# Kernel tuning notes

Measured on AMD Instinct MI355X. Metric: run time of the kernel, lower is better.

The kernel has to match this reference:

```python
import jax, jax.numpy as jnp
import numpy as np

HIDDEN = 4096
N_HEADS = 32
N_KV_HEADS = 8
HEAD_DIM = 128
ROPE_THETA = 1e6
RMS_EPS = 1e-6
SEQ = 2048


def setup_inputs() -> dict:
    key = jax.random.key(0)
    k1, k2, k3 = jax.random.split(key, 3)
    hidden_states = jax.random.normal(k1, (SEQ, HIDDEN), dtype=jnp.float32)
    # fused QKV weight: [hidden, (H + 2*Hkv) * head_dim]
    qkv_out = (N_HEADS + 2 * N_KV_HEADS) * HEAD_DIM
    w_qkv = jax.random.normal(k2, (HIDDEN, qkv_out), dtype=jnp.float32) * (HIDDEN ** -0.5)
    w_o = jax.random.normal(k3, (N_HEADS * HEAD_DIM, HIDDEN), dtype=jnp.float32) * ((N_HEADS * HEAD_DIM) ** -0.5)
    q_norm_w = jnp.ones((HEAD_DIM,), dtype=jnp.float32)
    k_norm_w = jnp.ones((HEAD_DIM,), dtype=jnp.float32)
    # NeoX-style rotary tables [T, head_dim/2]
    pos = jnp.arange(SEQ, dtype=jnp.float32)
    inv_freq = 1.0 / (ROPE_THETA ** (jnp.arange(0, HEAD_DIM, 2, dtype=jnp.float32) / HEAD_DIM))
    freqs = pos[:, None] * inv_freq[None, :]  # [T, d/2]
    cos = jnp.cos(freqs)
    sin = jnp.sin(freqs)
    return {"hidden_states": hidden_states, "cos": cos, "sin": sin,
            "w_qkv": w_qkv, "w_o": w_o, "q_norm_w": q_norm_w, "k_norm_w": k_norm_w}


def _rms_norm(x, w, eps=RMS_EPS):
    # per-head RMSNorm over last dim (head_dim)
    var = jnp.mean(jnp.square(x), axis=-1, keepdims=True)
    return x * jax.lax.rsqrt(var + eps) * w


def _rope(x, cos, sin):
    # NeoX rotate-half: x split into two halves of head_dim
    d2 = x.shape[-1] // 2
    x1, x2 = x[..., :d2], x[..., d2:]
    c = cos[:, None, :]  # [T,1,d/2] broadcast over heads
    s = sin[:, None, :]
    return jnp.concatenate([x1 * c - x2 * s, x2 * c + x1 * s], axis=-1)


def reference(hidden_states, cos, sin, w_qkv, w_o, q_norm_w, k_norm_w):
    T = hidden_states.shape[0]
    H, Hkv, D = N_HEADS, N_KV_HEADS, HEAD_DIM
    G = H // Hkv  # GQA group size
    scale = D ** -0.5

    qkv = hidden_states @ w_qkv  # [T, (H+2Hkv)*D]
    q, k, v = jnp.split(qkv, [H * D, (H + Hkv) * D], axis=1)
    q = q.reshape(T, H, D)
    k = k.reshape(T, Hkv, D)
    v = v.reshape(T, Hkv, D)

    q = _rms_norm(q, q_norm_w)
    k = _rms_norm(k, k_norm_w)
    q = _rope(q, cos, sin)
    k = _rope(k, cos, sin)

    # GQA: group query heads onto shared KV heads
    qg = q.reshape(T, Hkv, G, D)
    scores = jnp.einsum('qhgd,khd->hgqk', qg, k) * scale  # [Hkv,G,T,T]
    causal = jnp.tril(jnp.ones((T, T), dtype=bool))
    scores = jnp.where(causal, scores, jnp.float32(-1e30))
    probs = jax.nn.softmax(scores, axis=-1)
    out = jnp.einsum('hgqk,khd->qhgd', probs, v).reshape(T, H * D)
    return out @ w_o  # [T, hidden]
```

## Files before the change

kernel.cpp:

```cpp
#include <hip/hip_runtime.h>
#include <stdint.h>

#define SEQ   2048
#define HID   4096
#define NQH   32
#define NKVH  8
#define HD    128
#define QKVN  6144

typedef uint16_t u16;
typedef __attribute__((ext_vector_type(8))) short bf16x8;
typedef __attribute__((ext_vector_type(4))) float f32x4;
typedef __attribute__((ext_vector_type(4))) unsigned int u32x4;

static __device__ __forceinline__ float bf2f(u16 h){
  union { float f; unsigned int u; } v; v.u = ((unsigned int)h) << 16; return v.f;
}
static __device__ __forceinline__ u16 f2bf(float f){
  unsigned int u = __float_as_uint(f);
  return (u16)((u + 0x7fffu + ((u >> 16) & 1u)) >> 16);
}
static __device__ __forceinline__ f32x4 mfma16(bf16x8 a, bf16x8 b, f32x4 c){
  return __builtin_amdgcn_mfma_f32_16x16x32_bf16(a, b, c, 0, 0, 0);
}
static __device__ __forceinline__ void gload16(const void* g, void* l){
  __builtin_amdgcn_global_load_lds((const __attribute__((address_space(1))) void*)g,
                                   (__attribute__((address_space(3))) void*)l, 16, 0, 0);
}

__global__ void k_cvt(const float* __restrict__ src, u16* __restrict__ dst, int n4){
  int i = blockIdx.x * blockDim.x + threadIdx.x;
  if (i >= n4) return;
  float4 v = ((const float4*)src)[i];
  uint2 o;
  o.x = (unsigned)f2bf(v.x) | ((unsigned)f2bf(v.y) << 16);
  o.y = (unsigned)f2bf(v.z) | ((unsigned)f2bf(v.w) << 16);
  ((uint2*)dst)[i] = o;
}

__global__ void k_addf(const float* __restrict__ a, float* __restrict__ o, int n4){
  int i = blockIdx.x * blockDim.x + threadIdx.x;
  if (i >= n4) return;
  float4 x = ((const float4*)o)[i];
  float4 y = ((const float4*)a)[i];
  x.x += y.x; x.y += y.y; x.z += y.z; x.w += y.w;
  ((float4*)o)[i] = x;
}

__global__ void k_transpose_cvt(const float* __restrict__ src, u16* __restrict__ dst, int K, int N){
  __shared__ float t[32][33];
  int n0 = blockIdx.x * 32, k0 = blockIdx.y * 32;
  int tx = threadIdx.x, ty = threadIdx.y;
#pragma unroll
  for (int i = 0; i < 32; i += 8)
    t[ty + i][tx] = src[(size_t)(k0 + ty + i) * N + n0 + tx];
  __syncthreads();
#pragma unroll
  for (int i = 0; i < 32; i += 8)
    dst[(size_t)(n0 + ty + i) * K + k0 + tx] = f2bf(t[tx][ty + i]);
}

__global__ __launch_bounds__(512) void k_gemm192(const u16* __restrict__ A, const u16* __restrict__ Bt,
                                                 u16* __restrict__ Cv, int M, int N, int K){
  __shared__ __align__(16) u16 Asm[2][256][64];
  __shared__ __align__(16) u16 Bsm[2][192][64];
  const int tid = threadIdx.x, lane = tid & 63, wid = tid >> 6;
  const int wm = wid >> 2, wn = wid & 3;
  const int l16 = lane & 15, lhi = lane >> 4;
  const int rx = l16 & 7;
  const int bid = blockIdx.x;
  const int xcd = bid & 7, jj = bid >> 3;
  const size_t bcol = (size_t)(xcd * 4 + jj % 4) * 192;
  const size_t brow = (size_t)((jj / 4) & 7) * 256;

  const f32x4 vz = {0.f, 0.f, 0.f, 0.f};
  f32x4 acc[8][3];
#pragma unroll
  for (int m = 0; m < 8; m++)
#pragma unroll
    for (int n = 0; n < 3; n++) acc[m][n] = vz;

  const int srow = lane >> 3;
  const int sg   = (lane & 7) ^ srow;
  const u16* Ags = A  + (brow + wid*8 + srow) * (size_t)K + sg*8;
  const u16* Bgs = Bt + (bcol + wid*8 + srow) * (size_t)K + sg*8;
  const int NT = K >> 6, NU = NT >> 1;

#define FRA(buf, mi, kh) (*(const bf16x8*)&Asm[buf][wm*128 + (mi)*16 + l16][(((kh)*4 + lhi) ^ rx) << 3])
#define FRB(buf, ni, kh) (*(const bf16x8*)&Bsm[buf][wn*48 + (ni)*16 + l16][(((kh)*4 + lhi) ^ rx) << 3])
#define STG_A(tile, half) do{ if ((tile) < NT){                                  \
    const size_t ko_ = (size_t)((half)*128) * K + (size_t)(tile) * 64;           \
    gload16(Ags + ko_,                &Asm[(tile)&1][(half)*128 + wid*8][0]);     \
    gload16(Ags + ko_ + (size_t)64*K, &Asm[(tile)&1][(half)*128 + 64 + wid*8][0]); } }while(0)
#define STG_B(tile, r) do{ if ((tile) < NT){                                     \
    const size_t ko_ = (size_t)((r)*64) * K + (size_t)(tile) * 64;               \
    gload16(Bgs + ko_, &Bsm[(tile)&1][(r)*64 + wid*8][0]); } }while(0)

  STG_B(0,0); STG_B(0,1); STG_B(0,2);
  STG_A(0,0); STG_A(0,1);
  STG_B(1,0); STG_B(1,1); STG_B(1,2);
  asm volatile("s_waitcnt vmcnt(3)" ::: "memory");
  __builtin_amdgcn_sched_barrier(0);
  __builtin_amdgcn_s_barrier();

  bf16x8 fA[4][2], fB01[2][2], fB2[2];
  for (int u = 0; u < NU; ++u){
    const int t = 2 * u;
#pragma unroll
    for (int mi = 0; mi < 4; ++mi){ fA[mi][0] = FRA(0, mi, 0); fA[mi][1] = FRA(0, mi, 1); }
#pragma unroll
    for (int ni = 0; ni < 2; ++ni){ fB01[ni][0] = FRB(0, ni, 0); fB01[ni][1] = FRB(0, ni, 1); }
    STG_A(t + 1, 0);
    asm volatile("s_waitcnt lgkmcnt(8)" ::: "memory");
    __builtin_amdgcn_s_barrier();
    asm volatile("s_waitcnt lgkmcnt(0)" ::: "memory");
    __builtin_amdgcn_sched_barrier(0);
    __builtin_amdgcn_s_setprio(1);
#pragma unroll
    for (int kh = 0; kh < 2; ++kh)
#pragma unroll
      for (int mi = 0; mi < 4; ++mi)
#pragma unroll
        for (int ni = 0; ni < 2; ++ni)
          acc[mi][ni] = mfma16(fA[mi][kh], fB01[ni][kh], acc[mi][ni]);
    __builtin_amdgcn_s_setprio(0);
    __builtin_amdgcn_s_barrier();
    fB2[0] = FRB(0, 2, 0); fB2[1] = FRB(0, 2, 1);
    STG_A(t + 1, 1);
    __builtin_amdgcn_s_barrier();
    asm volatile("s_waitcnt lgkmcnt(0)" ::: "memory");
    __builtin_amdgcn_sched_barrier(0);
    __builtin_amdgcn_s_setprio(1);
#pragma unroll
    for (int kh = 0; kh < 2; ++kh)
#pragma unroll
      for (int mi = 0; mi < 4; ++mi)
        acc[mi][2] = mfma16(fA[mi][kh], fB2[kh], acc[mi][2]);
    __builtin_amdgcn_s_setprio(0);
    __builtin_amdgcn_s_barrier();
#pragma unroll
    for (int mi = 0; mi < 4; ++mi){ fA[mi][0] = FRA(0, 4 + mi, 0); fA[mi][1] = FRA(0, 4 + mi, 1); }
    STG_B(t + 2, 0);
    __builtin_amdgcn_s_barrier();
    asm volatile("s_waitcnt lgkmcnt(0)" ::: "memory");
    __builtin_amdgcn_sched_barrier(0);
    __builtin_amdgcn_s_setprio(1);
#pragma unroll
    for (int kh = 0; kh < 2; ++kh)
#pragma unroll
      for (int mi = 0; mi < 4; ++mi)
#pragma unroll
        for (int ni = 0; ni < 2; ++ni)
          acc[4 + mi][ni] = mfma16(fA[mi][kh], fB01[ni][kh], acc[4 + mi][ni]);
    __builtin_amdgcn_s_setprio(0);
    __builtin_amdgcn_s_barrier();
    STG_B(t + 2, 1); STG_B(t + 2, 2);
    __builtin_amdgcn_s_barrier();
    asm volatile("s_waitcnt lgkmcnt(0)" ::: "memory");
    __builtin_amdgcn_sched_barrier(0);
    __builtin_amdgcn_s_setprio(1);
#pragma unroll
    for (int kh = 0; kh < 2; ++kh)
#pragma unroll
      for (int mi = 0; mi < 4; ++mi)
        acc[4 + mi][2] = mfma16(fA[mi][kh], fB2[kh], acc[4 + mi][2]);
    __builtin_amdgcn_s_setprio(0);
    if (u == NU - 1) asm volatile("s_waitcnt vmcnt(0)" ::: "memory");
    else             asm volatile("s_waitcnt vmcnt(3)" ::: "memory");
    __builtin_amdgcn_sched_barrier(0);
    __builtin_amdgcn_s_barrier();
#pragma unroll
    for (int mi = 0; mi < 4; ++mi){ fA[mi][0] = FRA(1, mi, 0); fA[mi][1] = FRA(1, mi, 1); }
#pragma unroll
    for (int ni = 0; ni < 2; ++ni){ fB01[ni][0] = FRB(1, ni, 0); fB01[ni][1] = FRB(1, ni, 1); }
    STG_A(t + 2, 0);
    asm volatile("s_waitcnt lgkmcnt(8)" ::: "memory");
    __builtin_amdgcn_s_barrier();
    asm volatile("s_waitcnt lgkmcnt(0)" ::: "memory");
    __builtin_amdgcn_sched_barrier(0);
    __builtin_amdgcn_s_setprio(1);
#pragma unroll
    for (int kh = 0; kh < 2; ++kh)
#pragma unroll
      for (int mi = 0; mi < 4; ++mi)
#pragma unroll
        for (int ni = 0; ni < 2; ++ni)
          acc[mi][ni] = mfma16(fA[mi][kh], fB01[ni][kh], acc[mi][ni]);
    __builtin_amdgcn_s_setprio(0);
    __builtin_amdgcn_s_barrier();
    fB2[0] = FRB(1, 2, 0); fB2[1] = FRB(1, 2, 1);
    STG_A(t + 2, 1);
    __builtin_amdgcn_s_barrier();
    asm volatile("s_waitcnt lgkmcnt(0)" ::: "memory");
    __builtin_amdgcn_sched_barrier(0);
    __builtin_amdgcn_s_setprio(1);
#pragma unroll
    for (int kh = 0; kh < 2; ++kh)
#pragma unroll
      for (int mi = 0; mi < 4; ++mi)
        acc[mi][2] = mfma16(fA[mi][kh], fB2[kh], acc[mi][2]);
    __builtin_amdgcn_s_setprio(0);
    __builtin_amdgcn_s_barrier();
#pragma unroll
    for (int mi = 0; mi < 4; ++mi){ fA[mi][0] = FRA(1, 4 + mi, 0); fA[mi][1] = FRA(1, 4 + mi, 1); }
    STG_B(t + 3, 0);
    __builtin_amdgcn_s_barrier();
    asm volatile("s_waitcnt lgkmcnt(0)" ::: "memory");
    __builtin_amdgcn_sched_barrier(0);
    __builtin_amdgcn_s_setprio(1);
#pragma unroll
    for (int kh = 0; kh < 2; ++kh)
#pragma unroll
      for (int mi = 0; mi < 4; ++mi)
#pragma unroll
        for (int ni = 0; ni < 2; ++ni)
          acc[4 + mi][ni] = mfma16(fA[mi][kh], fB01[ni][kh], acc[4 + mi][ni]);
    __builtin_amdgcn_s_setprio(0);
    __builtin_amdgcn_s_barrier();
    STG_B(t + 3, 1); STG_B(t + 3, 2);
    __builtin_amdgcn_s_barrier();
    asm volatile("s_waitcnt lgkmcnt(0)" ::: "memory");
    __builtin_amdgcn_sched_barrier(0);
    __builtin_amdgcn_s_setprio(1);
#pragma unroll
    for (int kh = 0; kh < 2; ++kh)
#pragma unroll
      for (int mi = 0; mi < 4; ++mi)
        acc[4 + mi][2] = mfma16(fA[mi][kh], fB2[kh], acc[4 + mi][2]);
    __builtin_amdgcn_s_setprio(0);
    asm volatile("s_waitcnt vmcnt(3)" ::: "memory");
    __builtin_amdgcn_sched_barrier(0);
    __builtin_amdgcn_s_barrier();
  }
#undef FRA
#undef FRB
#undef STG_A
#undef STG_B

#pragma unroll
  for (int mi = 0; mi < 8; mi++)
#pragma unroll
    for (int ni = 0; ni < 3; ni++)
#pragma unroll
      for (int i = 0; i < 4; i++){
        size_t row = brow + wm*128 + mi*16 + lhi*4 + i;
        size_t col = bcol + wn*48 + ni*16 + l16;
        Cv[row * (size_t)N + col] = f2bf(acc[mi][ni][i]);
      }
}

template<int OUTBF, int SPLITK, int XBC, int NBY>
__global__ __launch_bounds__(512) void k_gemm(const u16* __restrict__ A, const u16* __restrict__ Bt,
                                              void* __restrict__ Cv0, void* __restrict__ Cv1,
                                              int M, int N, int K){
  __shared__ __align__(16) u16 Asm[2][2][128][64];
  __shared__ __align__(16) u16 Bsm[2][2][128][64];
  const int tid = threadIdx.x, lane = tid & 63, wid = tid >> 6;
  const int wm = wid >> 2, wn = wid & 3;
  const int l16 = lane & 15, lhi = lane >> 4;
  const int rx = l16 & 7;
  const int bid = blockIdx.x;
  const int xcd = bid & 7, jj = bid >> 3;
  const int bcol_i = xcd * XBC + jj % XBC;
  const int rest = jj / XBC;
  const int brow_i = rest % NBY;
  const int kz = (SPLITK > 1) ? (rest / NBY) : 0;
  const size_t brow = (size_t)brow_i * 256, bcol = (size_t)bcol_i * 256;
  const int kbeg = kz * (K / SPLITK);
  void* Cv = (kz == 0) ? Cv0 : Cv1;

  const f32x4 vz = {0.f, 0.f, 0.f, 0.f};
  f32x4 acc[8][4];
#pragma unroll
  for (int m = 0; m < 8; m++)
#pragma unroll
    for (int n = 0; n < 4; n++) acc[m][n] = vz;

  const int srow = lane >> 3;
  const int sg   = (lane & 7) ^ srow;
  const u16* Ags = A  + (brow + wid*8 + srow) * (size_t)K + sg*8 + kbeg;
  const u16* Bgs = Bt + (bcol + wid*8 + srow) * (size_t)K + sg*8 + kbeg;
  const int NT = (K / SPLITK) >> 6;
  const int NU = NT >> 1;

#define FRA(buf, mi, kh) (*(const bf16x8*)&Asm[buf][wm][(mi)*16 + l16][(((kh)*4 + lhi) ^ rx) << 3])
#define FRB(buf, ni, kh) (*(const bf16x8*)&Bsm[buf][wn >> 1][(wn & 1)*64 + (ni)*16 + l16][(((kh)*4 + lhi) ^ rx) << 3])
#define STG_A(tile, half) do{ if ((tile) < NT){                                  \
    const size_t ko_ = (size_t)((half)*128) * K + (size_t)(tile) * 64;           \
    gload16(Ags + ko_,                &Asm[(tile)&1][half][wid*8][0]);           \
    gload16(Ags + ko_ + (size_t)64*K, &Asm[(tile)&1][half][64 + wid*8][0]); } }while(0)
#define STG_B(tile, half) do{ if ((tile) < NT){                                  \
    const size_t ko_ = (size_t)((half)*128) * K + (size_t)(tile) * 64;           \
    gload16(Bgs + ko_,                &Bsm[(tile)&1][half][wid*8][0]);           \
    gload16(Bgs + ko_ + (size_t)64*K, &Bsm[(tile)&1][half][64 + wid*8][0]); } }while(0)

  STG_B(0, 0); STG_B(0, 1); STG_A(0, 0); STG_A(0, 1); STG_B(1, 0); STG_B(1, 1);
  asm volatile("s_waitcnt vmcnt(4)" ::: "memory");
  __builtin_amdgcn_sched_barrier(0);
  __builtin_amdgcn_s_barrier();

  bf16x8 fA[4][2], fB01[2][2], fB23[2][2];
  for (int u = 0; u < NU; ++u){
    const int t = 2 * u;
#pragma unroll
    for (int mi = 0; mi < 4; ++mi){ fA[mi][0] = FRA(0, mi, 0); fA[mi][1] = FRA(0, mi, 1); }
#pragma unroll
    for (int ni = 0; ni < 2; ++ni){ fB01[ni][0] = FRB(0, ni, 0); fB01[ni][1] = FRB(0, ni, 1); }
    STG_A(t + 1, 0);
    asm volatile("s_waitcnt lgkmcnt(8)" ::: "memory");
    __builtin_amdgcn_s_barrier();
    asm volatile("s_waitcnt lgkmcnt(0)" ::: "memory");
    __builtin_amdgcn_sched_barrier(0);
    __builtin_amdgcn_s_setprio(1);
#pragma unroll
    for (int kh = 0; kh < 2; ++kh)
#pragma unroll
      for (int mi = 0; mi < 4; ++mi)
#pragma unroll
        for (int ni = 0; ni < 2; ++ni)
          acc[mi][ni] = mfma16(fA[mi][kh], fB01[ni][kh], acc[mi][ni]);
    __builtin_amdgcn_s_setprio(0);
    __builtin_amdgcn_s_barrier();
#pragma unroll
    for (int ni = 0; ni < 2; ++ni){ fB23[ni][0] = FRB(0, 2 + ni, 0); fB23[ni][1] = FRB(0, 2 + ni, 1); }
    STG_A(t + 1, 1);
    __builtin_amdgcn_s_barrier();
    asm volatile("s_waitcnt lgkmcnt(0)" ::: "memory");
    __builtin_amdgcn_sched_barrier(0);
    __builtin_amdgcn_s_setprio(1);
#pragma unroll
    for (int kh = 0; kh < 2; ++kh)
#pragma unroll
      for (int mi = 0; mi < 4; ++mi)
#pragma unroll
        for (int ni = 0; ni < 2; ++ni)
          acc[mi][2 + ni] = mfma16(fA[mi][kh], fB23[ni][kh], acc[mi][2 + ni]);
    __builtin_amdgcn_s_setprio(0);
    __builtin_amdgcn_s_barrier();
#pragma unroll
    for (int mi = 0; mi < 4; ++mi){ fA[mi][0] = FRA(0, 4 + mi, 0); fA[mi][1] = FRA(0, 4 + mi, 1); }
    STG_B(t + 2, 0);
    __builtin_amdgcn_s_barrier();
    asm volatile("s_waitcnt lgkmcnt(0)" ::: "memory");
    __builtin_amdgcn_sched_barrier(0);
    __builtin_amdgcn_s_setprio(1);
#pragma unroll
    for (int kh = 0; kh < 2; ++kh)
#pragma unroll
      for (int mi = 0; mi < 4; ++mi)
#pragma unroll
        for (int ni = 0; ni < 2; ++ni)
          acc[4 + mi][ni] = mfma16(fA[mi][kh], fB01[ni][kh], acc[4 + mi][ni]);
    __builtin_amdgcn_s_setprio(0);
    __builtin_amdgcn_s_barrier();
    STG_B(t + 2, 1);
    __builtin_amdgcn_s_barrier();
    asm volatile("s_waitcnt lgkmcnt(0)" ::: "memory");
    __builtin_amdgcn_sched_barrier(0);
    __builtin_amdgcn_s_setprio(1);
#pragma unroll
    for (int kh = 0; kh < 2; ++kh)
#pragma unroll
      for (int mi = 0; mi < 4; ++mi)
#pragma unroll
        for (int ni = 0; ni < 2; ++ni)
          acc[4 + mi][2 + ni] = mfma16(fA[mi][kh], fB23[ni][kh], acc[4 + mi][2 + ni]);
    __builtin_amdgcn_s_setprio(0);
    if (u == NU - 1) asm volatile("s_waitcnt vmcnt(0)" ::: "memory");
    else             asm volatile("s_waitcnt vmcnt(4)" ::: "memory");
    __builtin_amdgcn_sched_barrier(0);
    __builtin_amdgcn_s_barrier();
#pragma unroll
    for (int mi = 0; mi < 4; ++mi){ fA[mi][0] = FRA(1, mi, 0); fA[mi][1] = FRA(1, mi, 1); }
#pragma unroll
    for (int ni = 0; ni < 2; ++ni){ fB01[ni][0] = FRB(1, ni, 0); fB01[ni][1] = FRB(1, ni, 1); }
    STG_A(t + 2, 0);
    asm volatile("s_waitcnt lgkmcnt(8)" ::: "memory");
    __builtin_amdgcn_s_barrier();
    asm volatile("s_waitcnt lgkmcnt(0)" ::: "memory");
    __builtin_amdgcn_sched_barrier(0);
    __builtin_amdgcn_s_setprio(1);
#pragma unroll
    for (int kh = 0; kh < 2; ++kh)
#pragma unroll
      for (int mi = 0; mi < 4; ++mi)
#pragma unroll
        for (int ni = 0; ni < 2; ++ni)
          acc[mi][ni] = mfma16(fA[mi][kh], fB01[ni][kh], acc[mi][ni]);
    __builtin_amdgcn_s_setprio(0);
    __builtin_amdgcn_s_barrier();
#pragma unroll
    for (int ni = 0; ni < 2; ++ni){ fB23[ni][0] = FRB(1, 2 + ni, 0); fB23[ni][1] = FRB(1, 2 + ni, 1); }
    STG_A(t + 2, 1);
    __builtin_amdgcn_s_barrier();
    asm volatile("s_waitcnt lgkmcnt(0)" ::: "memory");
    __builtin_amdgcn_sched_barrier(0);
    __builtin_amdgcn_s_setprio(1);
#pragma unroll
    for (int kh = 0; kh < 2; ++kh)
#pragma unroll
      for (int mi = 0; mi < 4; ++mi)
#pragma unroll
        for (int ni = 0; ni < 2; ++ni)
          acc[mi][2 + ni] = mfma16(fA[mi][kh], fB23[ni][kh], acc[mi][2 + ni]);
    __builtin_amdgcn_s_setprio(0);
    __builtin_amdgcn_s_barrier();
#pragma unroll
    for (int mi = 0; mi < 4; ++mi){ fA[mi][0] = FRA(1, 4 + mi, 0); fA[mi][1] = FRA(1, 4 + mi, 1); }
    STG_B(t + 3, 0);
    __builtin_amdgcn_s_barrier();
    asm volatile("s_waitcnt lgkmcnt(0)" ::: "memory");
    __builtin_amdgcn_sched_barrier(0);
    __builtin_amdgcn_s_setprio(1);
#pragma unroll
    for (int kh = 0; kh < 2; ++kh)
#pragma unroll
      for (int mi = 0; mi < 4; ++mi)
#pragma unroll
        for (int ni = 0; ni < 2; ++ni)
          acc[4 + mi][ni] = mfma16(fA[mi][kh], fB01[ni][kh], acc[4 + mi][ni]);
    __builtin_amdgcn_s_setprio(0);
    __builtin_amdgcn_s_barrier();
    STG_B(t + 3, 1);
    __builtin_amdgcn_s_barrier();
    asm volatile("s_waitcnt lgkmcnt(0)" ::: "memory");
    __builtin_amdgcn_sched_barrier(0);
    __builtin_amdgcn_s_setprio(1);
#pragma unroll
    for (int kh = 0; kh < 2; ++kh)
#pragma unroll
      for (int mi = 0; mi < 4; ++mi)
#pragma unroll
        for (int ni = 0; ni < 2; ++ni)
          acc[4 + mi][2 + ni] = mfma16(fA[mi][kh], fB23[ni][kh], acc[4 + mi][2 + ni]);
    __builtin_amdgcn_s_setprio(0);
    asm volatile("s_waitcnt vmcnt(4)" ::: "memory");
    __builtin_amdgcn_sched_barrier(0);
    __builtin_amdgcn_s_barrier();
  }
#undef FRA
#undef FRB
#undef STG_A
#undef STG_B

#pragma unroll
  for (int mi = 0; mi < 8; mi++)
#pragma unroll
    for (int ni = 0; ni < 4; ni++)
#pragma unroll
      for (int i = 0; i < 4; i++){
        size_t row = brow + wm*128 + mi*16 + lhi*4 + i;
        size_t col = bcol + wn*64 + ni*16 + l16;
        if (OUTBF) ((u16*)Cv)[row * (size_t)N + col] = f2bf(acc[mi][ni][i]);
        else       ((float*)Cv)[row * (size_t)N + col] = acc[mi][ni][i];
      }
}

__global__ __launch_bounds__(256) void k_rmsrope(const u16* __restrict__ qkv, const float* __restrict__ cosp,
                                                 const float* __restrict__ sinp, const float* __restrict__ qw,
                                                 const float* __restrict__ kw, u16* __restrict__ Qr,
                                                 u16* __restrict__ Kr){
  int t = blockIdx.x;
  int lane = threadIdx.x & 63, w = threadIdx.x >> 6;
  int hh = blockIdx.y * 4 + w;
  bool isq = hh < NQH;
  int hl = isq ? hh : hh - NQH;
  const u16* src = qkv + (size_t)t * QKVN + (isq ? hl * HD : NQH * HD + hl * HD);
  unsigned u = *(const unsigned*)(src + 2 * lane);
  float x0 = bf2f((u16)(u & 0xffffu)), x1 = bf2f((u16)(u >> 16));
  float ss = x0 * x0 + x1 * x1;
#pragma unroll
  for (int m = 1; m < 64; m <<= 1) ss += __shfl_xor(ss, m);
  float rs = rsqrtf(ss * (1.f / HD) + 1e-6f);
  const float* wp = isq ? qw : kw;
  float w0 = wp[2 * lane], w1 = wp[2 * lane + 1];
  float xn0 = x0 * rs * w0, xn1 = x1 * rs * w1;
  float p0 = __shfl_xor(xn0, 32), p1 = __shfl_xor(xn1, 32);
  int j0 = (2 * lane) & 63;
  float c0 = cosp[t * 64 + j0], c1 = cosp[t * 64 + j0 + 1];
  float s0 = sinp[t * 64 + j0], s1 = sinp[t * 64 + j0 + 1];
  float o0, o1;
  if (lane < 32){ o0 = xn0 * c0 - p0 * s0; o1 = xn1 * c1 - p1 * s1; }
  else          { o0 = xn0 * c0 + p0 * s0; o1 = xn1 * c1 + p1 * s1; }
  if (isq){ o0 *= 0.08838834764831845f; o1 *= 0.08838834764831845f; }
  u16* dst = isq ? (Qr + ((size_t)hl * SEQ + t) * HD) : (Kr + ((size_t)hl * SEQ + t) * HD);
  *(unsigned*)(dst + 2 * lane) = (unsigned)f2bf(o0) | ((unsigned)f2bf(o1) << 16);
}

__global__ void k_vt(const u16* __restrict__ qkv, u16* __restrict__ VT){
  __shared__ u16 t[32][33];
  int t0 = blockIdx.x * 32, d0 = blockIdx.y * 32, hv = blockIdx.z;
  int tx = threadIdx.x, ty = threadIdx.y;
#pragma unroll
  for (int i = 0; i < 32; i += 8)
    t[ty + i][tx] = qkv[(size_t)(t0 + ty + i) * QKVN + (NQH + NKVH) * HD + hv * HD + d0 + tx];
  __syncthreads();
#pragma unroll
  for (int i = 0; i < 32; i += 8)
    VT[((size_t)hv * HD + d0 + ty + i) * SEQ + t0 + tx] = t[tx][ty + i];
}

__global__ __launch_bounds__(512) void k_attn(const u16* __restrict__ Q, const u16* __restrict__ Kg,
                                              const u16* __restrict__ VTg, u16* __restrict__ AO){
  __shared__ __align__(16) u16 Ksm[2][128][128];
  __shared__ __align__(16) u16 Vsm[128][128];
  __shared__ __align__(16) u16 Psm[8][16][136];
  int tid = threadIdx.x, lane = tid & 63, wid = tid >> 6;
  int l16 = lane & 15, lhi = lane >> 4;
  int bid = blockIdx.x;
  int kvg = bid & 7, rr = bid >> 3;
  int J = 7 - (rr >> 2);
  int hq = kvg * 4 + (rr & 3);
  int qb = J * 256;
  const u16* Kh = Kg  + (size_t)kvg * SEQ * HD;
  const u16* Vh = VTg + (size_t)kvg * HD * SEQ;
  const u16* Qh = Q   + (size_t)hq * SEQ * HD;

  bf16x8 qf[2][4];
#pragma unroll
  for (int m = 0; m < 2; m++)
#pragma unroll
    for (int ks = 0; ks < 4; ks++)
      qf[m][ks] = *(const bf16x8*)(Qh + (size_t)(qb + wid*32 + m*16 + l16) * HD + ks*32 + lhi*8);

  const f32x4 vz = {0.f, 0.f, 0.f, 0.f};
  f32x4 o[2][8];
  float mrow[2][4], lrow[2][4];
#pragma unroll
  for (int m = 0; m < 2; m++){
#pragma unroll
    for (int n = 0; n < 8; n++) o[m][n] = vz;
#pragma unroll
    for (int i = 0; i < 4; i++){ mrow[m][i] = -1e30f; lrow[m][i] = 0.f; }
  }

  int rsub = lane >> 4, g = lane & 15;
  const u16 *Ks0, *Ks1, *Ks2, *Ks3, *Vs0, *Vs1, *Vs2, *Vs3;
  {
    int r0 = wid*16 + 0*4 + rsub, r1 = wid*16 + 1*4 + rsub;
    int r2 = wid*16 + 2*4 + rsub, r3 = wid*16 + 3*4 + rsub;
    Ks0 = Kh + (size_t)r0 * HD + ((g ^ (r0 & 7)) << 3);
    Ks1 = Kh + (size_t)r1 * HD + ((g ^ (r1 & 7)) << 3);
    Ks2 = Kh + (size_t)r2 * HD + ((g ^ (r2 & 7)) << 3);
    Ks3 = Kh + (size_t)r3 * HD + ((g ^ (r3 & 7)) << 3);
    Vs0 = Vh + (size_t)r0 * SEQ + ((g ^ (r0 & 7)) << 3);
    Vs1 = Vh + (size_t)r1 * SEQ + ((g ^ (r1 & 7)) << 3);
    Vs2 = Vh + (size_t)r2 * SEQ + ((g ^ (r2 & 7)) << 3);
    Vs3 = Vh + (size_t)r3 * SEQ + ((g ^ (r3 & 7)) << 3);
  }

  gload16(Ks0, &Ksm[0][wid*16 +  0][0]);
  gload16(Ks1, &Ksm[0][wid*16 +  4][0]);
  gload16(Ks2, &Ksm[0][wid*16 +  8][0]);
  gload16(Ks3, &Ksm[0][wid*16 + 12][0]);
  asm volatile("s_waitcnt vmcnt(0)" ::: "memory");
  __builtin_amdgcn_sched_barrier(0);
  __builtin_amdgcn_s_barrier();

  int ntr = 2*J + 2;
  int wbase = qb + wid*32;
  for (int t = 0; t < ntr; t++){
    int cur = t & 1, nxt = cur ^ 1;
    int kt0 = t << 7;
    bool pf = (t + 1 < ntr);
    gload16(Vs0 + kt0, &Vsm[wid*16 +  0][0]);
    gload16(Vs1 + kt0, &Vsm[wid*16 +  4][0]);
    gload16(Vs2 + kt0, &Vsm[wid*16 +  8][0]);
    gload16(Vs3 + kt0, &Vsm[wid*16 + 12][0]);
    if (pf){
      size_t ko = (size_t)(kt0 + 128) * HD;
      gload16(Ks0 + ko, &Ksm[nxt][wid*16 +  0][0]);
      gload16(Ks1 + ko, &Ksm[nxt][wid*16 +  4][0]);
      gload16(Ks2 + ko, &Ksm[nxt][wid*16 +  8][0]);
      gload16(Ks3 + ko, &Ksm[nxt][wid*16 + 12][0]);
    }
    bool act = (kt0 <= wbase + 31);
    f32x4 s[2][8];
    if (act){
#pragma unroll
      for (int m = 0; m < 2; m++)
#pragma unroll
        for (int n = 0; n < 8; n++) s[m][n] = vz;
      const u16* kbase = &Ksm[cur][0][0];
      __builtin_amdgcn_s_setprio(1);
#pragma unroll
      for (int n = 0; n < 8; n++){
        int row = n*16 + l16, rxk = row & 7;
#pragma unroll
        for (int ks = 0; ks < 4; ks++){
          bf16x8 kf = *(const bf16x8*)(kbase + row*128 + (((ks*4 + lhi) ^ rxk) << 3));
          s[0][n] = mfma16(qf[0][ks], kf, s[0][n]);
          s[1][n] = mfma16(qf[1][ks], kf, s[1][n]);
        }
      }
      __builtin_amdgcn_s_setprio(0);
      if (kt0 + 127 > wbase){
#pragma unroll
        for (int m = 0; m < 2; m++)
#pragma unroll
          for (int n = 0; n < 8; n++)
#pragma unroll
            for (int i = 0; i < 4; i++)
              if (kt0 + n*16 + l16 > wbase + m*16 + lhi*4 + i) s[m][n][i] = -1e30f;
      }
#pragma unroll
      for (int m = 0; m < 2; m++)
#pragma unroll
        for (int i = 0; i < 4; i++){
          float tm = fmaxf(fmaxf(fmaxf(s[m][0][i], s[m][1][i]), fmaxf(s[m][2][i], s[m][3][i])),
                           fmaxf(fmaxf(s[m][4][i], s[m][5][i]), fmaxf(s[m][6][i], s[m][7][i])));
          tm = fmaxf(tm, __shfl_xor(tm, 1));
          tm = fmaxf(tm, __shfl_xor(tm, 2));
          tm = fmaxf(tm, __shfl_xor(tm, 4));
          tm = fmaxf(tm, __shfl_xor(tm, 8));
          float nm = fmaxf(mrow[m][i], tm);
          float sc = __expf(mrow[m][i] - nm);
          mrow[m][i] = nm;
          float rsum = 0.f;
#pragma unroll
          for (int n = 0; n < 8; n++){
            float p = __expf(s[m][n][i] - nm);
            s[m][n][i] = p;
            rsum += p;
          }
          rsum += __shfl_xor(rsum, 1);
          rsum += __shfl_xor(rsum, 2);
          rsum += __shfl_xor(rsum, 4);
          rsum += __shfl_xor(rsum, 8);
          lrow[m][i] = lrow[m][i] * sc + rsum;
#pragma unroll
          for (int n = 0; n < 8; n++) o[m][n][i] *= sc;
        }
    }
    if (pf) asm volatile("s_waitcnt vmcnt(4)" ::: "memory");
    else    asm volatile("s_waitcnt vmcnt(0)" ::: "memory");
    __builtin_amdgcn_sched_barrier(0);
    __builtin_amdgcn_s_barrier();
    __builtin_amdgcn_sched_barrier(0);
    if (act){
      bf16x8 pa0[4], pa1[4];
#pragma unroll
      for (int n = 0; n < 8; n++)
#pragma unroll
        for (int i = 0; i < 4; i++)
          Psm[wid][lhi*4 + i][n*16 + l16] = f2bf(s[0][n][i]);
#pragma unroll
      for (int ksv = 0; ksv < 4; ksv++)
        pa0[ksv] = *(const bf16x8*)&Psm[wid][l16][ksv*32 + lhi*8];
      __builtin_amdgcn_sched_barrier(0);
#pragma unroll
      for (int n = 0; n < 8; n++)
#pragma unroll
        for (int i = 0; i < 4; i++)
          Psm[wid][lhi*4 + i][n*16 + l16] = f2bf(s[1][n][i]);
#pragma unroll
      for (int ksv = 0; ksv < 4; ksv++)
        pa1[ksv] = *(const bf16x8*)&Psm[wid][l16][ksv*32 + lhi*8];
      __builtin_amdgcn_s_setprio(1);
#pragma unroll
      for (int ksv = 0; ksv < 4; ksv++){
#pragma unroll
        for (int n = 0; n < 8; n++){
          int row = n*16 + l16;
          bf16x8 vb = *(const bf16x8*)(&Vsm[0][0] + row*128 + (((ksv*4 + lhi) ^ (row & 7)) << 3));
          o[0][n] = mfma16(pa0[ksv], vb, o[0][n]);
          o[1][n] = mfma16(pa1[ksv], vb, o[1][n]);
        }
      }
      __builtin_amdgcn_s_setprio(0);
    }
    asm volatile("s_waitcnt vmcnt(0)" ::: "memory");
    __builtin_amdgcn_sched_barrier(0);
    __builtin_amdgcn_s_barrier();
  }
#pragma unroll
  for (int m = 0; m < 2; m++){
    float inv[4];
#pragma unroll
    for (int i = 0; i < 4; i++) inv[i] = 1.f / lrow[m][i];
#pragma unroll
    for (int n = 0; n < 8; n++)
#pragma unroll
      for (int i = 0; i < 4; i++){
        int trow = wbase + m*16 + lhi*4 + i;
        AO[(size_t)trow * HID + hq * HD + n*16 + l16] = f2bf(o[m][n][i] * inv[i]);
      }
  }
}

extern "C" void kernel_launch(void* const* d_in, const int* in_sizes, int n_in,
                              void* d_out, int out_size, void* d_ws, size_t ws_size,
                              hipStream_t stream){
  const float* hs   = (const float*)d_in[0];
  const float* cosp = (const float*)d_in[1];
  const float* sinp = (const float*)d_in[2];
  const float* wqkv = (const float*)d_in[3];
  const float* wo   = (const float*)d_in[4];
  const float* qw   = (const float*)d_in[5];
  const float* kw   = (const float*)d_in[6];
  float* out = (float*)d_out;
  char* ws = (char*)d_ws;
  u16* XB    = (u16*)(ws + 0);
  u16* WQKVT = (u16*)(ws + 16777216);
  u16* WOT   = (u16*)(ws + 0);
  float* SCR = (float*)(ws + 33554432);
  u16* QKV   = (u16*)(ws + 67108864);
  u16* QR    = (u16*)(ws + 92274688);
  u16* KR    = (u16*)(ws + 109051904);
  u16* VTB   = (u16*)(ws + 113246208);
  u16* AOB   = (u16*)(ws + 117440512);

  k_cvt<<<(SEQ * HID / 4 + 255) / 256, 256, 0, stream>>>(hs, XB, SEQ * HID / 4);
  k_transpose_cvt<<<dim3(QKVN / 32, HID / 32), dim3(32, 8), 0, stream>>>(wqkv, WQKVT, HID, QKVN);
  k_gemm192<<<256, 512, 0, stream>>>(XB, WQKVT, QKV, SEQ, QKVN, HID);
  k_transpose_cvt<<<dim3(HID / 32, HID / 32), dim3(32, 8), 0, stream>>>(wo, WOT, HID, HID);
  k_rmsrope<<<dim3(SEQ, 10), 256, 0, stream>>>(QKV, cosp, sinp, qw, kw, QR, KR);
  k_vt<<<dim3(SEQ / 32, HD / 32, NKVH), dim3(32, 8), 0, stream>>>(QKV, VTB);
  k_attn<<<256, 512, 0, stream>>>(QR, KR, VTB, AOB);
  k_gemm<0, 2, 2, 8><<<256, 512, 0, stream>>>(AOB, WOT, out, SCR, SEQ, HID, HID);
  k_addf<<<SEQ * HID / 4 / 256, 256, 0, stream>>>(SCR, out, SEQ * HID / 4);
}
```

Before: 374.9 us.

## Halve attention query tile to 128 rows and launch 512 blocks

The attention kernel now gives each block 128 query rows (16 per wave) instead of 256, and the grid grows from 256 to 512 blocks. Causal work per block is more even, and every wave now works on every KV tile, so the per-wave active flag goes away. P is written to shared memory before the barrier. Each K/V tile loaded from global memory is now used by half as many query rows, so total K/V traffic roughly doubles and there are fewer MFMAs per loaded fragment.

```diff
diff --git a/kernel.cpp b/kernel.cpp
--- a/kernel.cpp
+++ b/kernel.cpp
@@ -509,30 +509,25 @@
   int l16 = lane & 15, lhi = lane >> 4;
   int bid = blockIdx.x;
   int kvg = bid & 7, rr = bid >> 3;
-  int J = 7 - (rr >> 2);
+  int J = 15 - (rr >> 2);
   int hq = kvg * 4 + (rr & 3);
-  int qb = J * 256;
+  int qb = J * 128;
   const u16* Kh = Kg  + (size_t)kvg * SEQ * HD;
   const u16* Vh = VTg + (size_t)kvg * HD * SEQ;
   const u16* Qh = Q   + (size_t)hq * SEQ * HD;
 
-  bf16x8 qf[2][4];
-#pragma unroll
-  for (int m = 0; m < 2; m++)
-#pragma unroll
-    for (int ks = 0; ks < 4; ks++)
-      qf[m][ks] = *(const bf16x8*)(Qh + (size_t)(qb + wid*32 + m*16 + l16) * HD + ks*32 + lhi*8);
+  bf16x8 qf[4];
+#pragma unroll
+  for (int ks = 0; ks < 4; ks++)
+    qf[ks] = *(const bf16x8*)(Qh + (size_t)(qb + wid*16 + l16) * HD + ks*32 + lhi*8);
 
   const f32x4 vz = {0.f, 0.f, 0.f, 0.f};
-  f32x4 o[2][8];
-  float mrow[2][4], lrow[2][4];
-#pragma unroll
-  for (int m = 0; m < 2; m++){
-#pragma unroll
-    for (int n = 0; n < 8; n++) o[m][n] = vz;
-#pragma unroll
-    for (int i = 0; i < 4; i++){ mrow[m][i] = -1e30f; lrow[m][i] = 0.f; }
-  }
+  f32x4 o[8];
+  float mrow[4], lrow[4];
+#pragma unroll
+  for (int n = 0; n < 8; n++) o[n] = vz;
+#pragma unroll
+  for (int i = 0; i < 4; i++){ mrow[i] = -1e30f; lrow[i] = 0.f; }
 
   int rsub = lane >> 4, g = lane & 15;
   const u16 *Ks0, *Ks1, *Ks2, *Ks3, *Vs0, *Vs1, *Vs2, *Vs3;
@@ -557,8 +552,8 @@
   __builtin_amdgcn_sched_barrier(0);
   __builtin_amdgcn_s_barrier();
 
-  int ntr = 2*J + 2;
-  int wbase = qb + wid*32;
+  int ntr = J + 1;
+  int wrow0 = qb + wid*16;
   for (int t = 0; t < ntr; t++){
     int cur = t & 1, nxt = cur ^ 1;
     int kt0 = t << 7;
@@ -574,118 +569,90 @@
       gload16(Ks2 + ko, &Ksm[nxt][wid*16 +  8][0]);
       gload16(Ks3 + ko, &Ksm[nxt][wid*16 + 12][0]);
     }
-    bool act = (kt0 <= wbase + 31);
-    f32x4 s[2][8];
-    if (act){
-#pragma unroll
-      for (int m = 0; m < 2; m++)
-#pragma unroll
-        for (int n = 0; n < 8; n++) s[m][n] = vz;
-      const u16* kbase = &Ksm[cur][0][0];
-      __builtin_amdgcn_s_setprio(1);
+    f32x4 s[8];
+#pragma unroll
+    for (int n = 0; n < 8; n++) s[n] = vz;
+    const u16* kbase = &Ksm[cur][0][0];
+    __builtin_amdgcn_s_setprio(1);
+#pragma unroll
+    for (int n = 0; n < 8; n++){
+      int row = n*16 + l16, rxk = row & 7;
+#pragma unroll
+      for (int ks = 0; ks < 4; ks++){
+        bf16x8 kf = *(const bf16x8*)(kbase + row*128 + (((ks*4 + lhi) ^ rxk) << 3));
+        s[n] = mfma16(qf[ks], kf, s[n]);
+      }
+    }
+    __builtin_amdgcn_s_setprio(0);
+    if (kt0 + 127 > wrow0){
+#pragma unroll
+      for (int n = 0; n < 8; n++)
+#pragma unroll
+        for (int i = 0; i < 4; i++)
+          if (kt0 + n*16 + l16 > wrow0 + lhi*4 + i) s[n][i] = -1e30f;
+    }
+#pragma unroll
+    for (int i = 0; i < 4; i++){
+      float tm = fmaxf(fmaxf(fmaxf(s[0][i], s[1][i]), fmaxf(s[2][i], s[3][i])),
+                       fmaxf(fmaxf(s[4][i], s[5][i]), fmaxf(s[6][i], s[7][i])));
+      tm = fmaxf(tm, __shfl_xor(tm, 1));
+      tm = fmaxf(tm, __shfl_xor(tm, 2));
+      tm = fmaxf(tm, __shfl_xor(tm, 4));
+      tm = fmaxf(tm, __shfl_xor(tm, 8));
+      float nm = fmaxf(mrow[i], tm);
+      float sc = __expf(mrow[i] - nm);
+      mrow[i] = nm;
+      float rsum = 0.f;
 #pragma unroll
       for (int n = 0; n < 8; n++){
-        int row = n*16 + l16, rxk = row & 7;
-#pragma unroll
-        for (int ks = 0; ks < 4; ks++){
-          bf16x8 kf = *(const bf16x8*)(kbase + row*128 + (((ks*4 + lhi) ^ rxk) << 3));
-          s[0][n] = mfma16(qf[0][ks], kf, s[0][n]);
-          s[1][n] = mfma16(qf[1][ks], kf, s[1][n]);
-        }
+        float p = __expf(s[n][i] - nm);
+        s[n][i] = p;
+        rsum += p;
       }
-      __builtin_amdgcn_s_setprio(0);
-      if (kt0 + 127 > wbase){
-#pragma unroll
-        for (int m = 0; m < 2; m++)
-#pragma unroll
-          for (int n = 0; n < 8; n++)
-#pragma unroll
-            for (int i = 0; i < 4; i++)
-              if (kt0 + n*16 + l16 > wbase + m*16 + lhi*4 + i) s[m][n][i] = -1e30f;
-      }
-#pragma unroll
-      for (int m = 0; m < 2; m++)
-#pragma unroll
-        for (int i = 0; i < 4; i++){
-          float tm = fmaxf(fmaxf(fmaxf(s[m][0][i], s[m][1][i]), fmaxf(s[m][2][i], s[m][3][i])),
-                           fmaxf(fmaxf(s[m][4][i], s[m][5][i]), fmaxf(s[m][6][i], s[m][7][i])));
-          tm = fmaxf(tm, __shfl_xor(tm, 1));
-          tm = fmaxf(tm, __shfl_xor(tm, 2));
-          tm = fmaxf(tm, __shfl_xor(tm, 4));
-          tm = fmaxf(tm, __shfl_xor(tm, 8));
-          float nm = fmaxf(mrow[m][i], tm);
-          float sc = __expf(mrow[m][i] - nm);
-          mrow[m][i] = nm;
-          float rsum = 0.f;
-#pragma unroll
-          for (int n = 0; n < 8; n++){
-            float p = __expf(s[m][n][i] - nm);
-            s[m][n][i] = p;
-            rsum += p;
-          }
-          rsum += __shfl_xor(rsum, 1);
-          rsum += __shfl_xor(rsum, 2);
-          rsum += __shfl_xor(rsum, 4);
-          rsum += __shfl_xor(rsum, 8);
-          lrow[m][i] = lrow[m][i] * sc + rsum;
-#pragma unroll
-          for (int n = 0; n < 8; n++) o[m][n][i] *= sc;
-        }
+      rsum += __shfl_xor(rsum, 1);
+      rsum += __shfl_xor(rsum, 2);
+      rsum += __shfl_xor(rsum, 4);
+      rsum += __shfl_xor(rsum, 8);
+      lrow[i] = lrow[i] * sc + rsum;
+#pragma unroll
+      for (int n = 0; n < 8; n++) o[n][i] *= sc;
     }
+#pragma unroll
+    for (int n = 0; n < 8; n++)
+#pragma unroll
+      for (int i = 0; i < 4; i++)
+        Psm[wid][lhi*4 + i][n*16 + l16] = f2bf(s[n][i]);
     if (pf) asm volatile("s_waitcnt vmcnt(4)" ::: "memory");
     else    asm volatile("s_waitcnt vmcnt(0)" ::: "memory");
     __builtin_amdgcn_sched_barrier(0);
     __builtin_amdgcn_s_barrier();
     __builtin_amdgcn_sched_barrier(0);
-    if (act){
-      bf16x8 pa0[4], pa1[4];
-#pragma unroll
-      for (int n = 0; n < 8; n++)
-#pragma unroll
-        for (int i = 0; i < 4; i++)
-          Psm[wid][lhi*4 + i][n*16 + l16] = f2bf(s[0][n][i]);
-#pragma unroll
-      for (int ksv = 0; ksv < 4; ksv++)
-        pa0[ksv] = *(const bf16x8*)&Psm[wid][l16][ksv*32 + lhi*8];
-      __builtin_amdgcn_sched_barrier(0);
-#pragma unroll
-      for (int n = 0; n < 8; n++)
-#pragma unroll
-        for (int i = 0; i < 4; i++)
-          Psm[wid][lhi*4 + i][n*16 + l16] = f2bf(s[1][n][i]);
-#pragma unroll
-      for (int ksv = 0; ksv < 4; ksv++)
-        pa1[ksv] = *(const bf16x8*)&Psm[wid][l16][ksv*32 + lhi*8];
-      __builtin_amdgcn_s_setprio(1);
-#pragma unroll
-      for (int ksv = 0; ksv < 4; ksv++){
-#pragma unroll
-        for (int n = 0; n < 8; n++){
-          int row = n*16 + l16;
-          bf16x8 vb = *(const bf16x8*)(&Vsm[0][0] + row*128 + (((ksv*4 + lhi) ^ (row & 7)) << 3));
-          o[0][n] = mfma16(pa0[ksv], vb, o[0][n]);
-          o[1][n] = mfma16(pa1[ksv], vb, o[1][n]);
-        }
+    __builtin_amdgcn_s_setprio(1);
+#pragma unroll
+    for (int ksv = 0; ksv < 4; ksv++){
+      bf16x8 pa = *(const bf16x8*)&Psm[wid][l16][ksv*32 + lhi*8];
+#pragma unroll
+      for (int n = 0; n < 8; n++){
+        int row = n*16 + l16;
+        bf16x8 vb = *(const bf16x8*)(&Vsm[0][0] + row*128 + (((ksv*4 + lhi) ^ (row & 7)) << 3));
+        o[n] = mfma16(pa, vb, o[n]);
       }
-      __builtin_amdgcn_s_setprio(0);
     }
+    __builtin_amdgcn_s_setprio(0);
     asm volatile("s_waitcnt vmcnt(0)" ::: "memory");
     __builtin_amdgcn_sched_barrier(0);
     __builtin_amdgcn_s_barrier();
   }
-#pragma unroll
-  for (int m = 0; m < 2; m++){
-    float inv[4];
-#pragma unroll
-    for (int i = 0; i < 4; i++) inv[i] = 1.f / lrow[m][i];
-#pragma unroll
-    for (int n = 0; n < 8; n++)
-#pragma unroll
-      for (int i = 0; i < 4; i++){
-        int trow = wbase + m*16 + lhi*4 + i;
-        AO[(size_t)trow * HID + hq * HD + n*16 + l16] = f2bf(o[m][n][i] * inv[i]);
-      }
-  }
+  float inv[4];
+#pragma unroll
+  for (int i = 0; i < 4; i++) inv[i] = 1.f / lrow[i];
+#pragma unroll
+  for (int n = 0; n < 8; n++)
+#pragma unroll
+    for (int i = 0; i < 4; i++){
+      int trow = wrow0 + lhi*4 + i;
+      AO[(size_t)trow * HID + hq * HD + n*16 + l16] = f2bf(o[n][i] * inv[i]);
+    }
 }
 
 extern "C" void kernel_launch(void* const* d_in, const int* in_sizes, int n_in,
@@ -716,7 +683,7 @@
   k_transpose_cvt<<<dim3(HID / 32, HID / 32), dim3(32, 8), 0, stream>>>(wo, WOT, HID, HID);
   k_rmsrope<<<dim3(SEQ, 10), 256, 0, stream>>>(QKV, cosp, sinp, qw, kw, QR, KR);
   k_vt<<<dim3(SEQ / 32, HD / 32, NKVH), dim3(32, 8), 0, stream>>>(QKV, VTB);
-  k_attn<<<256, 512, 0, stream>>>(QR, KR, VTB, AOB);
+  k_attn<<<512, 512, 0, stream>>>(QR, KR, VTB, AOB);
   k_gemm<0, 2, 2, 8><<<256, 512, 0, stream>>>(AOB, WOT, out, SCR, SEQ, HID, HID);
   k_addf<<<SEQ * HID / 4 / 256, 256, 0, stream>>>(SCR, out, SEQ * HID / 4);
 }
```

Result: faster. 339.0 us (-9.6%).
